# Kernel optimization log

Hardware: AMD Instinct MI355X
Metric: run time of the kernel (lower is better)

Reference implementation:

```python
import jax, jax.numpy as jnp
import numpy as np

B, S, D, P, N_IMGS = 64, 197, 768, 196, 50000  # S = P + 1 (class token)
GRID = float(np.sqrt(P))  # 14.0, matches np.sqrt(no_of_patches)


def setup_inputs() -> dict:
    key = jax.random.key(0)
    ks = jax.random.split(key, 12)
    x = jax.random.normal(ks[0], (B, S, D), dtype=jnp.float32)
    img_ids = jax.random.randint(ks[1], (B,), 0, N_IMGS, dtype=jnp.int32)
    mask = jnp.zeros((B, S), dtype=jnp.bool_)  # unused by the module's forward
    w = 0.02
    Wq = w * jax.random.normal(ks[2], (D, D), dtype=jnp.float32)
    bq = jnp.zeros((D,), dtype=jnp.float32)
    Wk = w * jax.random.normal(ks[3], (D, D), dtype=jnp.float32)
    bk = jnp.zeros((D,), dtype=jnp.float32)
    Wv = w * jax.random.normal(ks[4], (D, D), dtype=jnp.float32)
    bv = jnp.zeros((D,), dtype=jnp.float32)
    # per-image Gaussian params (init: avgs~0, std_devs=1 as in the module)
    avgs = 0.05 * jax.random.normal(ks[5], (N_IMGS, 2, P), dtype=jnp.float32)
    std_devs = jnp.ones((N_IMGS, 2, P), dtype=jnp.float32)
    # the torch code draws fresh N(0,1) noise per image inside forward; we
    # materialize it as an input for determinism: noise[:,0]=norm_x, noise[:,1]=norm_y
    noise = jax.random.normal(ks[6], (B, 2, P), dtype=jnp.float32)
    return {"x": x, "img_ids": img_ids, "mask": mask, "Wq": Wq, "bq": bq,
            "Wk": Wk, "bk": bk, "Wv": Wv, "bv": bv,
            "avgs": avgs, "std_devs": std_devs, "noise": noise}


def _gather(t, idx):
    # t: (B,S,D), idx: (B,P) -> (B,P,D)
    return jnp.take_along_axis(t, idx[:, :, None], axis=1)


def reference(x, img_ids, mask, Wq, bq, Wk, bk, Wv, bv, avgs, std_devs, noise):
    q = x @ Wq + bq
    k = x @ Wk + bk
    v = x @ Wv + bv

    a = avgs[img_ids]        # (B,2,P)
    s = std_devs[img_ids]    # (B,2,P)
    key_x = (noise[:, 0] - a[:, 0]) / s[:, 0]  # (B,P)
    key_y = (noise[:, 1] - a[:, 1]) / s[:, 1]

    x1, x2 = jnp.ceil(key_x), jnp.floor(key_x)
    y1, y2 = jnp.ceil(key_y), jnp.floor(key_y)

    def bilin(px, py):  # (1-|px-kx|)*(1-|py-ky|)
        return (1.0 - jnp.abs(px - key_x)) * (1.0 - jnp.abs(py - key_y))

    def idx(px, py):  # long-cast (truncation) of grid*y+x, wrapped like torch neg-indexing
        return (GRID * py + px).astype(jnp.int32) % S

    w11, w21, w12, w22 = bilin(x1, y1), bilin(x2, y1), bilin(x1, y2), bilin(x2, y2)
    i11, i21, i12, i22 = idx(x1, y1), idx(x2, y1), idx(x1, y2), idx(x2, y2)

    def sample(t):  # bilinear 4-point gather -> (B,P,D)
        return (w11[:, :, None] * _gather(t, i11)
                + w21[:, :, None] * _gather(t, i21)
                + w12[:, :, None] * _gather(t, i12)
                + w22[:, :, None] * _gather(t, i22))

    sk = sample(k)
    sv = sample(v)

    cls = jnp.ones((x.shape[0], 1, D), dtype=x.dtype)  # class_emb = ones(1,1,D)
    sk = jnp.concatenate([cls, sk], axis=1)  # (B,S,D)
    sv = jnp.concatenate([cls, sv], axis=1)  # (B,S,D)

    # at_sc[b,s] = <sampled_key[b,s], q[b,s]>; original shape (S,1,1) per image,
    # softmax over the singleton dim (faithful to F.softmax(at_sc, dim=1))
    scores = jnp.einsum('bsd,bsd->bs', sk, q)[:, :, None]  # (B,S,1)
    attn = jax.nn.softmax(scores, axis=-1)                 # ones (singleton axis)
    out = attn * sv                                        # (B,S,D)
    return out
```

## Files before the change

kernel.cpp:

```cpp
#include <hip/hip_runtime.h>
#include <cstdint>
#include <cstddef>

#define Bb 64
#define Ss 197
#define Dd 768
#define Pp 196

typedef short bf16x8 __attribute__((ext_vector_type(8)));
typedef short bf16x4 __attribute__((ext_vector_type(4)));
typedef float f32x4  __attribute__((ext_vector_type(4)));
struct alignas(16) F4 { float v[4]; };

__device__ __forceinline__ int mod_s(int v) {
    int r = v % Ss;
    return (r < 0) ? r + Ss : r;
}

__device__ __forceinline__ unsigned short f2bf(float f) {
    union { float f; unsigned u; } v; v.f = f;
    unsigned r = (v.u + 0x7FFFu + ((v.u >> 16) & 1u)) >> 16;
    return (unsigned short)r;
}

struct GParams {
    float w0, w1, w2, w3;
    int i0, i1, i2, i3;
};

__device__ __forceinline__ GParams gather_params(
    const int* img_ids, const float* avgs, const float* stds,
    const float* noise, int b, int p)
{
    const int id = img_ids[b];
    const float a0 = avgs [((size_t)id * 2    ) * Pp + p];
    const float a1 = avgs [((size_t)id * 2 + 1) * Pp + p];
    const float s0 = stds [((size_t)id * 2    ) * Pp + p];
    const float s1 = stds [((size_t)id * 2 + 1) * Pp + p];
    const float nx = noise[((size_t)b  * 2    ) * Pp + p];
    const float ny = noise[((size_t)b  * 2 + 1) * Pp + p];
    const float kx = (nx - a0) / s0;
    const float ky = (ny - a1) / s1;
    const float cx = ceilf(kx),  fx = floorf(kx);
    const float cy = ceilf(ky),  fy = floorf(ky);
    const float dcx = 1.0f - fabsf(cx - kx);
    const float dfx = 1.0f - fabsf(fx - kx);
    const float dcy = 1.0f - fabsf(cy - ky);
    const float dfy = 1.0f - fabsf(fy - ky);
    GParams g;
    g.w0 = dcx * dcy;  g.w1 = dfx * dcy;  g.w2 = dcx * dfy;  g.w3 = dfx * dfy;
    g.i0 = mod_s((int)(14.0f * cy + cx));
    g.i1 = mod_s((int)(14.0f * cy + fx));
    g.i2 = mod_s((int)(14.0f * fy + cx));
    g.i3 = mod_s((int)(14.0f * fy + fx));
    return g;
}

#define GATHER_BLKS 3136
#define TRANS_BLKS  144
#define CLS_BLKS    192

__global__ __launch_bounds__(256) void gsa_prep(
    const float* __restrict__ x,
    const int*   __restrict__ img_ids,
    const float* __restrict__ Wv,
    const float* __restrict__ avgs,
    const float* __restrict__ stds,
    const float* __restrict__ noise,
    unsigned short* __restrict__ Ag,
    unsigned short* __restrict__ WvT,
    float* __restrict__ wsB,
    float* __restrict__ out)
{
    __shared__ short T[64][66];
    const int t   = threadIdx.x;
    const int blk = blockIdx.x;

    if (blk < GATHER_BLKS) {
        const int lane = t & 63;
        const int w    = t >> 6;
        const int m    = blk * 4 + w;
        const int b    = m / Pp;
        const int p    = m - b * Pp;
        GParams g = gather_params(img_ids, avgs, stds, noise, b, p);
        const size_t xb = (size_t)b * Ss;
        const float* r0 = x + (xb + g.i0) * Dd;
        const float* r1 = x + (xb + g.i1) * Dd;
        const float* r2 = x + (xb + g.i2) * Dd;
        const float* r3 = x + (xb + g.i3) * Dd;
        unsigned short* dst = Ag + (size_t)m * Dd;
        #pragma unroll
        for (int c = 0; c < 3; ++c) {
            const int k = c * 256 + lane * 4;
            F4 v0 = *reinterpret_cast<const F4*>(r0 + k);
            F4 v1 = *reinterpret_cast<const F4*>(r1 + k);
            F4 v2 = *reinterpret_cast<const F4*>(r2 + k);
            F4 v3 = *reinterpret_cast<const F4*>(r3 + k);
            bf16x4 o;
            #pragma unroll
            for (int q = 0; q < 4; ++q)
                o[q] = (short)f2bf(g.w0*v0.v[q] + g.w1*v1.v[q] + g.w2*v2.v[q] + g.w3*v3.v[q]);
            *reinterpret_cast<bf16x4*>(dst + k) = o;
        }
        if (lane == 0) wsB[m] = g.w0 + g.w1 + g.w2 + g.w3;
    } else if (blk < GATHER_BLKS + TRANS_BLKS) {
        const int tb = blk - GATHER_BLKS;
        const int k0 = (tb % 12) * 64;
        const int n0 = (tb / 12) * 64;
        const int tx = t & 63, tyy = t >> 6;
        #pragma unroll
        for (int pass = 0; pass < 16; ++pass) {
            const int i = pass * 4 + tyy;
            T[i][tx] = (short)f2bf(Wv[(size_t)(k0 + i) * Dd + n0 + tx]);
        }
        __syncthreads();
        #pragma unroll
        for (int pass = 0; pass < 16; ++pass) {
            const int n = pass * 4 + tyy;
            WvT[(size_t)(n0 + n) * Dd + k0 + tx] = (unsigned short)T[tx][n];
        }
    } else {
        const int idx = (blk - GATHER_BLKS - TRANS_BLKS) * 256 + t;
        const int b = idx / Dd;
        const int d = idx - b * Dd;
        out[(size_t)b * Ss * Dd + d] = 1.0f;
    }
}

__global__ __launch_bounds__(256, 2) void gsa_gemm2(
    const unsigned short* __restrict__ Ag,
    const unsigned short* __restrict__ WvT,
    const float* __restrict__ wsB,
    const float* __restrict__ bv,
    float* __restrict__ out)
{
    const int t    = threadIdx.x;
    const int m0   = blockIdx.x * 128;
    const int n0   = blockIdx.y * 128;
    const int lane = t & 63;
    const int wv   = t >> 6;
    const int col  = lane & 15;
    const int quad = lane >> 4;
    const int wm   = (wv & 1) * 64;
    const int wn   = (wv >> 1) * 64;

    const unsigned short* ap[4];
    const unsigned short* bp[4];
    #pragma unroll
    for (int mi = 0; mi < 4; ++mi)
        ap[mi] = Ag + (size_t)(m0 + wm + mi * 16 + col) * Dd + quad * 8;
    #pragma unroll
    for (int ni = 0; ni < 4; ++ni)
        bp[ni] = WvT + (size_t)(n0 + wn + ni * 16 + col) * Dd + quad * 8;

    f32x4 acc[4][4];
    #pragma unroll
    for (int i = 0; i < 4; ++i)
        #pragma unroll
        for (int j = 0; j < 4; ++j) acc[i][j] = (f32x4)0.0f;

    bf16x8 aC[4], bC[4];
    #pragma unroll
    for (int mi = 0; mi < 4; ++mi) aC[mi] = *reinterpret_cast<const bf16x8*>(ap[mi]);
    #pragma unroll
    for (int ni = 0; ni < 4; ++ni) bC[ni] = *reinterpret_cast<const bf16x8*>(bp[ni]);

    #pragma unroll 2
    for (int kt = 32; kt <= Dd; kt += 32) {
        bf16x8 aN[4], bN[4];
        if (kt < Dd) {
            #pragma unroll
            for (int mi = 0; mi < 4; ++mi) aN[mi] = *reinterpret_cast<const bf16x8*>(ap[mi] + kt);
            #pragma unroll
            for (int ni = 0; ni < 4; ++ni) bN[ni] = *reinterpret_cast<const bf16x8*>(bp[ni] + kt);
        }
        #pragma unroll
        for (int mi = 0; mi < 4; ++mi)
            #pragma unroll
            for (int ni = 0; ni < 4; ++ni)
                acc[mi][ni] = __builtin_amdgcn_mfma_f32_16x16x32_bf16(
                    aC[mi], bC[ni], acc[mi][ni], 0, 0, 0);
        #pragma unroll
        for (int mi = 0; mi < 4; ++mi) aC[mi] = aN[mi];
        #pragma unroll
        for (int ni = 0; ni < 4; ++ni) bC[ni] = bN[ni];
    }

    float bvv[4];
    #pragma unroll
    for (int ni = 0; ni < 4; ++ni) bvv[ni] = bv[n0 + wn + ni * 16 + col];

    #pragma unroll
    for (int mi = 0; mi < 4; ++mi) {
        #pragma unroll
        for (int rg = 0; rg < 4; ++rg) {
            const int mg = m0 + wm + mi * 16 + quad * 4 + rg;
            const int b  = mg / Pp;
            const float wsv = wsB[mg];
            float* orow = out + ((size_t)(mg + b + 1)) * Dd;
            #pragma unroll
            for (int ni = 0; ni < 4; ++ni)
                orow[n0 + wn + ni * 16 + col] = acc[mi][ni][rg] + wsv * bvv[ni];
        }
    }
}

__global__ __launch_bounds__(256) void wv_transpose(
    const float* __restrict__ Wv, unsigned short* __restrict__ WvT)
{
    const int u = blockIdx.x * 256 + threadIdx.x;
    const int o = u * 8;
    const int n = o / Dd;
    const int k = o - n * Dd;
    bf16x8 tv;
    #pragma unroll
    for (int j = 0; j < 8; ++j) tv[j] = (short)f2bf(Wv[(size_t)(k + j) * Dd + n]);
    *reinterpret_cast<bf16x8*>(WvT + o) = tv;
}

__global__ __launch_bounds__(256) void gsa_fill_cls(float* __restrict__ out) {
    const int idx = blockIdx.x * 256 + threadIdx.x;
    if (idx < Bb * Dd) {
        const int b = idx / Dd;
        const int d = idx - b * Dd;
        out[(size_t)b * Ss * Dd + d] = 1.0f;
    }
}

__global__ __launch_bounds__(256, 2) void gsa_mfma(
    const float* __restrict__ x, const int* __restrict__ img_ids,
    const unsigned short* __restrict__ WvT, const float* __restrict__ bv,
    const float* __restrict__ avgs, const float* __restrict__ stds,
    const float* __restrict__ noise, float* __restrict__ out)
{
    __shared__ short As[128][40];
    __shared__ short Bs[128][40];
    __shared__ float wsums[128];
    const int t  = threadIdx.x;
    const int m0 = blockIdx.x * 128;
    const int n0 = blockIdx.y * 128;
    const int r  = t >> 1;
    const int kh = t & 1;
    const int ko = kh * 16;
    float w0, w1, w2, w3;
    const float *sA0, *sA1, *sA2, *sA3;
    {
        const int m = m0 + r, b = m / Pp, p = m - b * Pp;
        GParams g = gather_params(img_ids, avgs, stds, noise, b, p);
        w0 = g.w0; w1 = g.w1; w2 = g.w2; w3 = g.w3;
        const size_t xb = (size_t)b * Ss;
        sA0 = x + (xb + g.i0) * Dd + ko;
        sA1 = x + (xb + g.i1) * Dd + ko;
        sA2 = x + (xb + g.i2) * Dd + ko;
        sA3 = x + (xb + g.i3) * Dd + ko;
        if (kh == 0) wsums[r] = w0 + w1 + w2 + w3;
    }
    const unsigned short* srcB = WvT + (size_t)(n0 + r) * Dd + ko;
    const int lane = t & 63, wv = t >> 6;
    const int col = lane & 15, quad = lane >> 4;
    const int wm = (wv & 1) * 64, wn = (wv >> 1) * 64;
    const short* aptr[4];
    const short* bptr[4];
    #pragma unroll
    for (int mi = 0; mi < 4; ++mi) aptr[mi] = &As[wm + mi * 16 + col][quad * 8];
    #pragma unroll
    for (int ni = 0; ni < 4; ++ni) bptr[ni] = &Bs[wn + ni * 16 + col][quad * 8];
    f32x4 acc[4][4];
    #pragma unroll
    for (int i = 0; i < 4; ++i)
        #pragma unroll
        for (int j = 0; j < 4; ++j) acc[i][j] = (f32x4)0.0f;
    #pragma unroll 1
    for (int kt = 0; kt < Dd; kt += 32) {
        F4 l0[4], l1[4], l2[4], l3[4];
        #pragma unroll
        for (int c = 0; c < 4; ++c) {
            l0[c] = *reinterpret_cast<const F4*>(sA0 + kt + c * 4);
            l1[c] = *reinterpret_cast<const F4*>(sA1 + kt + c * 4);
            l2[c] = *reinterpret_cast<const F4*>(sA2 + kt + c * 4);
            l3[c] = *reinterpret_cast<const F4*>(sA3 + kt + c * 4);
        }
        bf16x8 b0 = *reinterpret_cast<const bf16x8*>(srcB + kt);
        bf16x8 b1 = *reinterpret_cast<const bf16x8*>(srcB + kt + 8);
        bf16x8 ua0, ua1;
        #pragma unroll
        for (int e = 0; e < 8; ++e) {
            const int c = e >> 2, q = e & 3;
            ua0[e] = (short)f2bf(w0*l0[c].v[q] + w1*l1[c].v[q] + w2*l2[c].v[q] + w3*l3[c].v[q]);
        }
        #pragma unroll
        for (int e = 0; e < 8; ++e) {
            const int c = (e + 8) >> 2, q = e & 3;
            ua1[e] = (short)f2bf(w0*l0[c].v[q] + w1*l1[c].v[q] + w2*l2[c].v[q] + w3*l3[c].v[q]);
        }
        __syncthreads();
        *reinterpret_cast<bf16x8*>(&As[r][ko])     = ua0;
        *reinterpret_cast<bf16x8*>(&As[r][ko + 8]) = ua1;
        *reinterpret_cast<bf16x8*>(&Bs[r][ko])     = b0;
        *reinterpret_cast<bf16x8*>(&Bs[r][ko + 8]) = b1;
        __syncthreads();
        bf16x8 aF[4], bF[4];
        #pragma unroll
        for (int mi = 0; mi < 4; ++mi) aF[mi] = *reinterpret_cast<const bf16x8*>(aptr[mi]);
        #pragma unroll
        for (int ni = 0; ni < 4; ++ni) bF[ni] = *reinterpret_cast<const bf16x8*>(bptr[ni]);
        #pragma unroll
        for (int mi = 0; mi < 4; ++mi)
            #pragma unroll
            for (int ni = 0; ni < 4; ++ni)
                acc[mi][ni] = __builtin_amdgcn_mfma_f32_16x16x32_bf16(
                    aF[mi], bF[ni], acc[mi][ni], 0, 0, 0);
    }
    float bvv[4];
    #pragma unroll
    for (int ni = 0; ni < 4; ++ni) bvv[ni] = bv[n0 + wn + ni * 16 + col];
    #pragma unroll
    for (int mi = 0; mi < 4; ++mi) {
        #pragma unroll
        for (int rg = 0; rg < 4; ++rg) {
            const int ml = wm + mi * 16 + quad * 4 + rg;
            const int mg = m0 + ml;
            const int b  = mg / Pp;
            const float wsv = wsums[ml];
            float* orow = out + ((size_t)(mg + b + 1)) * Dd;
            #pragma unroll
            for (int ni = 0; ni < 4; ++ni)
                orow[n0 + wn + ni * 16 + col] = acc[mi][ni][rg] + wsv * bvv[ni];
        }
    }
}

extern "C" void kernel_launch(void* const* d_in, const int* in_sizes, int n_in,
                              void* d_out, int out_size, void* d_ws, size_t ws_size,
                              hipStream_t stream) {
    const float* x       = (const float*)d_in[0];
    const int*   img_ids = (const int*)  d_in[1];
    const float* Wv      = (const float*)d_in[7];
    const float* bv      = (const float*)d_in[8];
    const float* avgs    = (const float*)d_in[9];
    const float* stds    = (const float*)d_in[10];
    const float* noise   = (const float*)d_in[11];
    float* out = (float*)d_out;

    const size_t ag_bytes  = (size_t)Bb * Pp * Dd * sizeof(unsigned short);
    const size_t wvt_bytes = (size_t)Dd * Dd * sizeof(unsigned short);
    const size_t ws_need   = ag_bytes + wvt_bytes + (size_t)Bb * Pp * sizeof(float);

    if (d_ws != nullptr && ws_size >= ws_need) {
        unsigned short* Ag  = (unsigned short*)d_ws;
        unsigned short* WvT = (unsigned short*)((char*)d_ws + ag_bytes);
        float*          wsB = (float*)((char*)d_ws + ag_bytes + wvt_bytes);
        gsa_prep<<<GATHER_BLKS + TRANS_BLKS + CLS_BLKS, 256, 0, stream>>>(
            x, img_ids, Wv, avgs, stds, noise, Ag, WvT, wsB, out);
        dim3 grid((Bb * Pp) / 128, Dd / 128);
        gsa_gemm2<<<grid, 256, 0, stream>>>(Ag, WvT, wsB, bv, out);
    } else {
        unsigned short* WvT = (unsigned short*)d_ws;
        gsa_fill_cls<<<(Bb * Dd + 255) / 256, 256, 0, stream>>>(out);
        wv_transpose<<<(Dd * Dd / 8) / 256, 256, 0, stream>>>(Wv, WvT);
        dim3 grid((Bb * Pp) / 128, Dd / 128);
        gsa_mfma<<<grid, 256, 0, stream>>>(x, img_ids, WvT, bv, avgs, stds, noise, out);
    }
}
```

Baseline: 257.9 us.

## Stage GEMM tiles through double-buffered LDS with direct global-to-LDS loads

Replaces the register-prefetch GEMM, where each wave loaded its A/B fragments straight from global memory, with a kernel that stages 128x64 A and B tiles into double-buffered, XOR-swizzled LDS using global_load_lds. Waves then read their MFMA fragments from LDS. The grid becomes 1D with an XCD-aware remapping so that the blocks sharing an M tile land on the same XCD for L2 reuse. The aim is to cut redundant global traffic and improve cache locality, at the cost of 64KB of LDS per block and a barrier every k-stage.

```diff
diff --git a/kernel.cpp b/kernel.cpp
--- a/kernel.cpp
+++ b/kernel.cpp
@@ -21,6 +21,12 @@
     union { float f; unsigned u; } v; v.f = f;
     unsigned r = (v.u + 0x7FFFu + ((v.u >> 16) & 1u)) >> 16;
     return (unsigned short)r;
+}
+
+__device__ __forceinline__ void gload_lds16(const void* g, void* l) {
+    __builtin_amdgcn_global_load_lds(
+        (const __attribute__((address_space(1))) unsigned int*)g,
+        (__attribute__((address_space(3))) unsigned int*)l, 16, 0, 0);
 }
 
 struct GParams {
@@ -127,31 +133,59 @@
     }
 }
 
-__global__ __launch_bounds__(256, 2) void gsa_gemm2(
+#define NSTG 12
+
+__global__ __launch_bounds__(256, 2) void gsa_gemm4(
     const unsigned short* __restrict__ Ag,
     const unsigned short* __restrict__ WvT,
     const float* __restrict__ wsB,
     const float* __restrict__ bv,
     float* __restrict__ out)
 {
-    const int t    = threadIdx.x;
-    const int m0   = blockIdx.x * 128;
-    const int n0   = blockIdx.y * 128;
+    __shared__ short lds[2][16384];
+
+    const int t = threadIdx.x;
+    const int L      = blockIdx.x;
+    const int xcd    = L & 7;
+    const int grp    = L >> 3;
+    const int n_t    = grp % 6;
+    const int mchunk = grp / 6;
+    const int m_tile = mchunk * 8 + xcd;
+    if (m_tile >= 98) return;
+    const int m0 = m_tile * 128;
+    const int n0 = n_t * 128;
+
     const int lane = t & 63;
-    const int wv   = t >> 6;
+    const int w    = t >> 6;
+
+    const unsigned short* aSrc[4];
+    const unsigned short* bSrc[4];
+    int ldsA[4], ldsB[4];
+    #pragma unroll
+    for (int i = 0; i < 4; ++i) {
+        const int rr = (w * 4 + i) * 8 + (lane >> 3);
+        const int qq = (lane & 7) ^ (rr & 7);
+        aSrc[i] = Ag  + (size_t)(m0 + rr) * Dd + qq * 8;
+        bSrc[i] = WvT + (size_t)(n0 + rr) * Dd + qq * 8;
+        ldsA[i] = (w * 4 + i) * 512;
+        ldsB[i] = 8192 + (w * 4 + i) * 512;
+    }
+
     const int col  = lane & 15;
     const int quad = lane >> 4;
-    const int wm   = (wv & 1) * 64;
-    const int wn   = (wv >> 1) * 64;
-
-    const unsigned short* ap[4];
-    const unsigned short* bp[4];
-    #pragma unroll
-    for (int mi = 0; mi < 4; ++mi)
-        ap[mi] = Ag + (size_t)(m0 + wm + mi * 16 + col) * Dd + quad * 8;
-    #pragma unroll
-    for (int ni = 0; ni < 4; ++ni)
-        bp[ni] = WvT + (size_t)(n0 + wn + ni * 16 + col) * Dd + quad * 8;
+    const int wm   = (w & 1) * 64;
+    const int wn   = (w >> 1) * 64;
+    int offA[4][2], offB[4][2];
+    #pragma unroll
+    for (int i = 0; i < 4; ++i) {
+        const int ra = wm + i * 16 + col;
+        const int rb = wn + i * 16 + col;
+        #pragma unroll
+        for (int ks = 0; ks < 2; ++ks) {
+            offA[i][ks] = (ra * 8 + ((ks * 4 + quad) ^ (ra & 7))) * 8;
+            offB[i][ks] = 8192 + (rb * 8 + ((ks * 4 + quad) ^ (rb & 7))) * 8;
+        }
+    }
 
     f32x4 acc[4][4];
     #pragma unroll
@@ -159,31 +193,41 @@
         #pragma unroll
         for (int j = 0; j < 4; ++j) acc[i][j] = (f32x4)0.0f;
 
-    bf16x8 aC[4], bC[4];
-    #pragma unroll
-    for (int mi = 0; mi < 4; ++mi) aC[mi] = *reinterpret_cast<const bf16x8*>(ap[mi]);
-    #pragma unroll
-    for (int ni = 0; ni < 4; ++ni) bC[ni] = *reinterpret_cast<const bf16x8*>(bp[ni]);
-
-    #pragma unroll 2
-    for (int kt = 32; kt <= Dd; kt += 32) {
-        bf16x8 aN[4], bN[4];
-        if (kt < Dd) {
-            #pragma unroll
-            for (int mi = 0; mi < 4; ++mi) aN[mi] = *reinterpret_cast<const bf16x8*>(ap[mi] + kt);
-            #pragma unroll
-            for (int ni = 0; ni < 4; ++ni) bN[ni] = *reinterpret_cast<const bf16x8*>(bp[ni] + kt);
-        }
-        #pragma unroll
-        for (int mi = 0; mi < 4; ++mi)
+    #pragma unroll
+    for (int i = 0; i < 4; ++i) {
+        gload_lds16(aSrc[i], &lds[0][ldsA[i]]);
+        gload_lds16(bSrc[i], &lds[0][ldsB[i]]);
+    }
+    __syncthreads();
+
+    for (int s = 0; s < NSTG; ++s) {
+        if (s + 1 < NSTG) {
+            const int kadv = (s + 1) * 64;
+            short* nbuf = lds[(s + 1) & 1];
+            #pragma unroll
+            for (int i = 0; i < 4; ++i) {
+                gload_lds16(aSrc[i] + kadv, &nbuf[ldsA[i]]);
+                gload_lds16(bSrc[i] + kadv, &nbuf[ldsB[i]]);
+            }
+        }
+        const short* base = lds[s & 1];
+        #pragma unroll
+        for (int ks = 0; ks < 2; ++ks) {
+            bf16x8 aF[4], bF[4];
+            #pragma unroll
+            for (int mi = 0; mi < 4; ++mi)
+                aF[mi] = *reinterpret_cast<const bf16x8*>(base + offA[mi][ks]);
             #pragma unroll
             for (int ni = 0; ni < 4; ++ni)
-                acc[mi][ni] = __builtin_amdgcn_mfma_f32_16x16x32_bf16(
-                    aC[mi], bC[ni], acc[mi][ni], 0, 0, 0);
-        #pragma unroll
-        for (int mi = 0; mi < 4; ++mi) aC[mi] = aN[mi];
-        #pragma unroll
-        for (int ni = 0; ni < 4; ++ni) bC[ni] = bN[ni];
+                bF[ni] = *reinterpret_cast<const bf16x8*>(base + offB[ni][ks]);
+            #pragma unroll
+            for (int mi = 0; mi < 4; ++mi)
+                #pragma unroll
+                for (int ni = 0; ni < 4; ++ni)
+                    acc[mi][ni] = __builtin_amdgcn_mfma_f32_16x16x32_bf16(
+                        aF[mi], bF[ni], acc[mi][ni], 0, 0, 0);
+        }
+        __syncthreads();
     }
 
     float bvv[4];
@@ -352,8 +396,7 @@
         float*          wsB = (float*)((char*)d_ws + ag_bytes + wvt_bytes);
         gsa_prep<<<GATHER_BLKS + TRANS_BLKS + CLS_BLKS, 256, 0, stream>>>(
             x, img_ids, Wv, avgs, stds, noise, Ag, WvT, wsB, out);
-        dim3 grid((Bb * Pp) / 128, Dd / 128);
-        gsa_gemm2<<<grid, 256, 0, stream>>>(Ag, WvT, wsB, bv, out);
+        gsa_gemm4<<<624, 256, 0, stream>>>(Ag, WvT, wsB, bv, out);
     } else {
         unsigned short* WvT = (unsigned short*)d_ws;
         gsa_fill_cls<<<(Bb * Dd + 255) / 256, 256, 0, stream>>>(out);
```

After: 215.5 us. 16.4% less time.
